# Kernel tuning notes

Hardware: AMD Instinct MI355X
Metric: run time of the kernel (lower is better)

Reference implementation:

```python
import jax, jax.numpy as jnp
import numpy as np

H = 768
L = 9
M = 5            # max_span_length
CTX_RATIO = 0.5
NEG_INF = -1e30


def setup_inputs() -> dict:
    key = jax.random.key(0)
    ks = jax.random.split(key, 12)
    B, S = 4, 2048
    sc = 1.0 / np.sqrt(H)
    return {
        "sequence_output": jax.random.normal(ks[0], (B, S, H), dtype=jnp.float32),
        "Wc": jax.random.normal(ks[1], (H, L), dtype=jnp.float32) * sc,
        "bc": jnp.zeros((L,), dtype=jnp.float32),
        "wa": jax.random.normal(ks[2], (H,), dtype=jnp.float32) * sc,
        "ba": jnp.zeros((), dtype=jnp.float32),
        "W1": jax.random.normal(ks[3], (2 * H, H), dtype=jnp.float32) * (1.0 / np.sqrt(2 * H)),
        "b1": jnp.zeros((H,), dtype=jnp.float32),
        "gamma": jnp.ones((H,), dtype=jnp.float32),
        "beta": jnp.zeros((H,), dtype=jnp.float32),
        "W2": jax.random.normal(ks[4], (H, L), dtype=jnp.float32) * sc,
        "b2": jnp.zeros((L,), dtype=jnp.float32),
    }


def reference(sequence_output, Wc, bc, wa, ba, W1, b1, gamma, beta, W2, b2):
    x = sequence_output                        # [B,S,H]
    B, S, _ = x.shape
    base_logits = jnp.einsum('bsh,hl->bsl', x, Wc) + bc   # [B,S,L]

    # sliding-window indices: window [i-M, i+M] clipped to [0, S)
    offsets = jnp.arange(-M, M + 1)            # [W]
    idx = jnp.arange(S)[:, None] + offsets     # [S,W]
    valid = (idx >= 0) & (idx < S)             # [S,W]
    idx_c = jnp.clip(idx, 0, S - 1)            # [S,W]

    # attention scores over window (span_attention linear -> scalar per token)
    scores = jnp.einsum('bsh,h->bs', x, wa) + ba           # [B,S]
    win_scores = scores[:, idx_c]                          # [B,S,W]
    win_scores = jnp.where(valid[None], win_scores, NEG_INF)
    attn = jax.nn.softmax(win_scores, axis=-1)             # [B,S,W]

    win_tokens = x[:, idx_c]                               # [B,S,W,H] gather
    weighted_ctx = jnp.einsum('bsw,bswh->bsh', attn, win_tokens)

    token_with_ctx = jnp.concatenate([x, weighted_ctx], axis=-1)  # [B,S,2H]
    h = jnp.einsum('bsd,dh->bsh', token_with_ctx, W1) + b1
    # LayerNorm (eps = 1e-5, torch default)
    mu = jnp.mean(h, axis=-1, keepdims=True)
    var = jnp.mean((h - mu) ** 2, axis=-1, keepdims=True)
    h = (h - mu) * jax.lax.rsqrt(var + 1e-5) * gamma + beta
    h = jax.nn.gelu(h, approximate=False)                  # torch nn.GELU default (erf)
    ctx_logits = jnp.einsum('bsh,hl->bsl', h, W2) + b2

    return (1.0 - CTX_RATIO) * base_logits + CTX_RATIO * ctx_logits
```

## Files before the change

### kernel.cpp

```cpp
#include <hip/hip_runtime.h>
#include <hip/hip_bf16.h>
#include <math.h>

#define S_LEN 2048
#define BATCH 4
#define HDIM 768
#define LOUT 9
#define NROWS (BATCH*S_LEN)
#define K2H 1536
#define WIN 11
#define NEG_INF_F (-1e30f)

typedef __attribute__((ext_vector_type(4))) float f32x4;
typedef __attribute__((ext_vector_type(8))) short bf16x8;

static __device__ __forceinline__ void async_ld16(const void* g, void* l) {
  __builtin_amdgcn_global_load_lds((const __attribute__((address_space(1))) void*)g,
                                   (__attribute__((address_space(3))) void*)l, 16, 0, 0);
}

static __device__ __forceinline__ unsigned short f2bf(float f) {
  union { float f; unsigned int u; } v; v.f = f;
  unsigned int u = v.u;
  unsigned int r = (u + 0x7fffu + ((u >> 16) & 1u)) >> 16;
  return (unsigned short)r;
}

__global__ __launch_bounds__(192) void k_prep(const float* __restrict__ x,
                                              const float* __restrict__ wa,
                                              const float* __restrict__ ba,
                                              unsigned short* __restrict__ xc,
                                              float* __restrict__ scores) {
  __shared__ float red[3];
  int row = blockIdx.x;
  int t = threadIdx.x;
  int lane = t & 63, wave = t >> 6;
  const float4 v = *(const float4*)(x + row * HDIM + t * 4);
  const float4 w = *(const float4*)(wa + t * 4);
  ushort4 o;
  o.x = f2bf(v.x); o.y = f2bf(v.y); o.z = f2bf(v.z); o.w = f2bf(v.w);
  *(ushort4*)(xc + row * K2H + t * 4) = o;
  float p = v.x * w.x + v.y * w.y + v.z * w.z + v.w * w.w;
  #pragma unroll
  for (int m = 1; m < 64; m <<= 1) p += __shfl_xor(p, m);
  if (lane == 0) red[wave] = p;
  __syncthreads();
  if (t == 0) scores[row] = red[0] + red[1] + red[2] + ba[0];
}

__global__ __launch_bounds__(256) void k_prep_w1t(const float* __restrict__ W1,
                                                  unsigned short* __restrict__ W1t) {
  __shared__ float tile[32][33];
  int bk = blockIdx.x % 48;
  int bn = blockIdx.x / 48;
  int tc = threadIdx.x % 32;
  int tr = threadIdx.x / 32;
  #pragma unroll
  for (int i = 0; i < 32; i += 8) {
    tile[tr + i][tc] = W1[(bk*32 + tr + i) * HDIM + bn*32 + tc];
  }
  __syncthreads();
  #pragma unroll
  for (int i = 0; i < 32; i += 8) {
    W1t[(bn*32 + tr + i) * K2H + bk*32 + tc] = f2bf(tile[tc][tr + i]);
  }
}

__global__ __launch_bounds__(256) void k_ctx(const float* __restrict__ x,
                                             const float* __restrict__ scores,
                                             const float* __restrict__ Wc,
                                             const float* __restrict__ bc,
                                             unsigned short* __restrict__ xc,
                                             float* __restrict__ base) {
  __shared__ float scl[WIN];
  __shared__ float es[WIN];
  __shared__ int rowidx[WIN];
  __shared__ float red[4][LOUT];
  int row = blockIdx.x;
  int b = row >> 11, s = row & 2047;
  int t = threadIdx.x;
  if (t < WIN) {
    int j = s - 5 + t;
    bool valid = (j >= 0) && (j < S_LEN);
    int jc = valid ? j : (j < 0 ? 0 : S_LEN - 1);
    rowidx[t] = b * S_LEN + jc;
    scl[t] = valid ? scores[b * S_LEN + jc] : NEG_INF_F;
  }
  __syncthreads();
  float mx = scl[0];
  #pragma unroll
  for (int w = 1; w < WIN; ++w) mx = fmaxf(mx, scl[w]);
  if (t < WIN) {
    float sv = scl[t];
    es[t] = (sv > -1e29f) ? __expf(sv - mx) : 0.f;
  }
  __syncthreads();
  float ssum = 0.f;
  #pragma unroll
  for (int w = 0; w < WIN; ++w) ssum += es[w];
  float inv = 1.f / ssum;
  float acc0 = 0.f, acc1 = 0.f, acc2 = 0.f;
  #pragma unroll
  for (int w = 0; w < WIN; ++w) {
    float aw = es[w] * inv;
    const float* xr = x + rowidx[w] * HDIM;
    acc0 += aw * xr[t];
    acc1 += aw * xr[t + 256];
    acc2 += aw * xr[t + 512];
  }
  unsigned short* dst = xc + row * K2H + HDIM;
  dst[t]       = f2bf(acc0);
  dst[t + 256] = f2bf(acc1);
  dst[t + 512] = f2bf(acc2);
  const float* xr = x + row * HDIM;
  float p[LOUT] = {};
  #pragma unroll
  for (int i = 0; i < 3; ++i) {
    int e = t + i * 256;
    float xv = xr[e];
    const float* wrow = Wc + e * LOUT;
    #pragma unroll
    for (int l = 0; l < LOUT; ++l) p[l] += xv * wrow[l];
  }
  #pragma unroll
  for (int l = 0; l < LOUT; ++l) {
    #pragma unroll
    for (int m = 1; m < 64; m <<= 1) p[l] += __shfl_xor(p[l], m);
  }
  int lane = t & 63, wave = t >> 6;
  if (lane == 0) {
    #pragma unroll
    for (int l = 0; l < LOUT; ++l) red[wave][l] = p[l];
  }
  __syncthreads();
  if (t < LOUT) {
    base[row * LOUT + t] = red[0][t] + red[1][t] + red[2][t] + red[3][t] + bc[t];
  }
}

__global__ __launch_bounds__(256) void k_gemm(const unsigned short* __restrict__ A,
                                              const unsigned short* __restrict__ Bt,
                                              const float* __restrict__ b1,
                                              float* __restrict__ Hout) {
  __shared__ unsigned short As[2][128 * 64];
  __shared__ unsigned short Bs[2][64 * 64];
  int bid = blockIdx.x;
  int obid = (bid & 7) * 96 + (bid >> 3);
  int bm = obid / 12, bn = obid % 12;
  int t = threadIdx.x;
  int lane = t & 63, wave = t >> 6;
  int rsub = lane >> 3;
  int kslot = lane & 7;

  int aRow0 = bm * 128 + (wave * 4 + 0) * 8 + rsub;
  int bRow0 = bn * 64  + (wave * 2 + 0) * 8 + rsub;
  const unsigned short* gA = A  + aRow0 * K2H + kslot * 8;
  const unsigned short* gB = Bt + bRow0 * K2H + kslot * 8;

  f32x4 acc[2][4] = {};
  int laneRow = lane & 15;
  int laneK = (lane >> 4) * 8;
  const unsigned short* aBase0 = &As[0][(wave * 32 + laneRow) * 64 + laneK];
  const unsigned short* bBase0 = &Bs[0][laneRow * 64 + laneK];

#define STAGE(buf, kt) do {                                                   \
    _Pragma("unroll")                                                         \
    for (int j = 0; j < 4; ++j)                                               \
      async_ld16(gA + j * 8 * K2H + (kt), &As[buf][(wave * 4 + j) * 512]);    \
    _Pragma("unroll")                                                         \
    for (int j = 0; j < 2; ++j)                                               \
      async_ld16(gB + j * 8 * K2H + (kt), &Bs[buf][(wave * 2 + j) * 512]);    \
  } while (0)

#define COMPUTE(buf) do {                                                     \
    const unsigned short* aB = aBase0 + (buf) * 128 * 64;                     \
    const unsigned short* bB = bBase0 + (buf) * 64 * 64;                      \
    _Pragma("unroll")                                                         \
    for (int kk = 0; kk < 2; ++kk) {                                          \
      bf16x8 af[2], bf[4];                                                    \
      _Pragma("unroll")                                                       \
      for (int m = 0; m < 2; ++m) af[m] = *(const bf16x8*)(aB + m*16*64 + kk*32); \
      _Pragma("unroll")                                                       \
      for (int n = 0; n < 4; ++n) bf[n] = *(const bf16x8*)(bB + n*16*64 + kk*32); \
      _Pragma("unroll")                                                       \
      for (int m = 0; m < 2; ++m)                                             \
        _Pragma("unroll")                                                     \
        for (int n = 0; n < 4; ++n)                                           \
          acc[m][n] = __builtin_amdgcn_mfma_f32_16x16x32_bf16(af[m], bf[n], acc[m][n], 0, 0, 0); \
    }                                                                         \
  } while (0)

  STAGE(0, 0);
  __syncthreads();
  int cur = 0;
  for (int kt = 64; kt < K2H; kt += 64) {
    STAGE(cur ^ 1, kt);
    COMPUTE(cur);
    __syncthreads();
    cur ^= 1;
  }
  COMPUTE(cur);

  int orow = bm * 128 + wave * 32 + (lane >> 4) * 4;
  int ocol = bn * 64 + (lane & 15);
  #pragma unroll
  for (int m = 0; m < 2; ++m)
    #pragma unroll
    for (int n = 0; n < 4; ++n) {
      int col = ocol + n * 16;
      float bv = b1[col];
      #pragma unroll
      for (int r = 0; r < 4; ++r) {
        Hout[(orow + m * 16 + r) * HDIM + col] = acc[m][n][r] + bv;
      }
    }
#undef STAGE
#undef COMPUTE
}

__global__ __launch_bounds__(256) void k_ln(const float* __restrict__ Hin,
                                            const float* __restrict__ gamma,
                                            const float* __restrict__ beta,
                                            const float* __restrict__ W2,
                                            const float* __restrict__ b2,
                                            const float* __restrict__ base,
                                            float* __restrict__ out) {
  __shared__ float redS[4], redQ[4], redp[4][LOUT];
  int row = blockIdx.x;
  int t = threadIdx.x;
  int lane = t & 63, wave = t >> 6;
  const float* hr = Hin + row * HDIM;
  float v0 = hr[t], v1 = hr[t + 256], v2 = hr[t + 512];
  float s1 = v0 + v1 + v2;
  float s2 = v0 * v0 + v1 * v1 + v2 * v2;
  #pragma unroll
  for (int m = 1; m < 64; m <<= 1) { s1 += __shfl_xor(s1, m); s2 += __shfl_xor(s2, m); }
  if (lane == 0) { redS[wave] = s1; redQ[wave] = s2; }
  __syncthreads();
  s1 = redS[0] + redS[1] + redS[2] + redS[3];
  s2 = redQ[0] + redQ[1] + redQ[2] + redQ[3];
  float mu = s1 * (1.f / HDIM);
  float var = s2 * (1.f / HDIM) - mu * mu;
  float rstd = rsqrtf(var + 1e-5f);
  float p[LOUT] = {};
  float vv[3] = { v0, v1, v2 };
  #pragma unroll
  for (int i = 0; i < 3; ++i) {
    int e = t + i * 256;
    float g = (vv[i] - mu) * rstd * gamma[e] + beta[e];
    float gg = 0.5f * g * (1.f + erff(g * 0.70710678118654752f));
    const float* wrow = W2 + e * LOUT;
    #pragma unroll
    for (int l = 0; l < LOUT; ++l) p[l] += gg * wrow[l];
  }
  #pragma unroll
  for (int l = 0; l < LOUT; ++l) {
    #pragma unroll
    for (int m = 1; m < 64; m <<= 1) p[l] += __shfl_xor(p[l], m);
  }
  if (lane == 0) {
    #pragma unroll
    for (int l = 0; l < LOUT; ++l) redp[wave][l] = p[l];
  }
  __syncthreads();
  if (t < LOUT) {
    float cl = redp[0][t] + redp[1][t] + redp[2][t] + redp[3][t] + b2[t];
    out[row * LOUT + t] = 0.5f * base[row * LOUT + t] + 0.5f * cl;
  }
}

extern "C" void kernel_launch(void* const* d_in, const int* in_sizes, int n_in,
                              void* d_out, int out_size, void* d_ws, size_t ws_size,
                              hipStream_t stream) {
  const float* x     = (const float*)d_in[0];
  const float* Wc    = (const float*)d_in[1];
  const float* bc    = (const float*)d_in[2];
  const float* wa    = (const float*)d_in[3];
  const float* ba    = (const float*)d_in[4];
  const float* W1    = (const float*)d_in[5];
  const float* b1    = (const float*)d_in[6];
  const float* gamma = (const float*)d_in[7];
  const float* beta  = (const float*)d_in[8];
  const float* W2    = (const float*)d_in[9];
  const float* b2    = (const float*)d_in[10];
  float* out = (float*)d_out;

  char* ws = (char*)d_ws;
  unsigned short* xc  = (unsigned short*)(ws);
  unsigned short* w1t = (unsigned short*)(ws + 25165824);
  float* scores       = (float*)(ws + 27525120);
  float* base         = (float*)(ws + 27557888);
  float* hbuf         = (float*)(ws + 27852800);

  k_prep    <<<dim3(8192), dim3(192), 0, stream>>>(x, wa, ba, xc, scores);
  k_prep_w1t<<<dim3(1152), dim3(256), 0, stream>>>(W1, w1t);
  k_ctx     <<<dim3(8192), dim3(256), 0, stream>>>(x, scores, Wc, bc, xc, base);
  k_gemm    <<<dim3(768),  dim3(256), 0, stream>>>(xc, w1t, b1, hbuf);
  k_ln      <<<dim3(8192), dim3(256), 0, stream>>>(hbuf, gamma, beta, W2, b2, base, out);
}
```

Measured before the change: 194.5 us.

## Fuse score computation into context kernel and retile GEMM with swizzled K=32 stages

Removes the separate prep kernel by having each context block recompute the window attention scores from its 11 loaded rows and also write the bf16 copy of x. This drops a launch and the scores round trip, at the cost of redundant dot products (11x per row) and cross-wave reductions. The GEMM now stages K in 32-wide chunks with an XOR-swizzled LDS layout to avoid bank conflicts. Halving the LDS footprint with launch bounds of 4 blocks per CU aims for higher occupancy, but the K loop now runs twice as many iterations with a barrier each.

```diff
diff --git a/kernel.cpp b/kernel.cpp
--- a/kernel.cpp
+++ b/kernel.cpp
@@ -26,28 +26,6 @@
   return (unsigned short)r;
 }
 
-__global__ __launch_bounds__(192) void k_prep(const float* __restrict__ x,
-                                              const float* __restrict__ wa,
-                                              const float* __restrict__ ba,
-                                              unsigned short* __restrict__ xc,
-                                              float* __restrict__ scores) {
-  __shared__ float red[3];
-  int row = blockIdx.x;
-  int t = threadIdx.x;
-  int lane = t & 63, wave = t >> 6;
-  const float4 v = *(const float4*)(x + row * HDIM + t * 4);
-  const float4 w = *(const float4*)(wa + t * 4);
-  ushort4 o;
-  o.x = f2bf(v.x); o.y = f2bf(v.y); o.z = f2bf(v.z); o.w = f2bf(v.w);
-  *(ushort4*)(xc + row * K2H + t * 4) = o;
-  float p = v.x * w.x + v.y * w.y + v.z * w.z + v.w * w.w;
-  #pragma unroll
-  for (int m = 1; m < 64; m <<= 1) p += __shfl_xor(p, m);
-  if (lane == 0) red[wave] = p;
-  __syncthreads();
-  if (t == 0) scores[row] = red[0] + red[1] + red[2] + ba[0];
-}
-
 __global__ __launch_bounds__(256) void k_prep_w1t(const float* __restrict__ W1,
                                                   unsigned short* __restrict__ W1t) {
   __shared__ float tile[32][33];
@@ -67,133 +45,155 @@
 }
 
 __global__ __launch_bounds__(256) void k_ctx(const float* __restrict__ x,
-                                             const float* __restrict__ scores,
+                                             const float* __restrict__ wa,
+                                             const float* __restrict__ ba,
                                              const float* __restrict__ Wc,
                                              const float* __restrict__ bc,
                                              unsigned short* __restrict__ xc,
                                              float* __restrict__ base) {
-  __shared__ float scl[WIN];
-  __shared__ float es[WIN];
-  __shared__ int rowidx[WIN];
-  __shared__ float red[4][LOUT];
+  __shared__ float sred[4][WIN];
+  __shared__ float redp[4][LOUT];
   int row = blockIdx.x;
   int b = row >> 11, s = row & 2047;
   int t = threadIdx.x;
-  if (t < WIN) {
-    int j = s - 5 + t;
+  int lane = t & 63, wave = t >> 6;
+
+  float xv[WIN][3];
+  bool vld[WIN];
+  #pragma unroll
+  for (int w = 0; w < WIN; ++w) {
+    int j = s - 5 + w;
     bool valid = (j >= 0) && (j < S_LEN);
+    vld[w] = valid;
     int jc = valid ? j : (j < 0 ? 0 : S_LEN - 1);
-    rowidx[t] = b * S_LEN + jc;
-    scl[t] = valid ? scores[b * S_LEN + jc] : NEG_INF_F;
-  }
-  __syncthreads();
-  float mx = scl[0];
-  #pragma unroll
-  for (int w = 1; w < WIN; ++w) mx = fmaxf(mx, scl[w]);
-  if (t < WIN) {
-    float sv = scl[t];
-    es[t] = (sv > -1e29f) ? __expf(sv - mx) : 0.f;
-  }
-  __syncthreads();
-  float ssum = 0.f;
-  #pragma unroll
-  for (int w = 0; w < WIN; ++w) ssum += es[w];
+    const float* xr = x + (b * S_LEN + jc) * HDIM;
+    xv[w][0] = xr[t];
+    xv[w][1] = xr[t + 256];
+    xv[w][2] = xr[t + 512];
+  }
+  float wa0 = wa[t], wa1 = wa[t + 256], wa2 = wa[t + 512];
+
+  float sp[WIN];
+  #pragma unroll
+  for (int w = 0; w < WIN; ++w)
+    sp[w] = xv[w][0] * wa0 + xv[w][1] * wa1 + xv[w][2] * wa2;
+  #pragma unroll
+  for (int w = 0; w < WIN; ++w)
+    #pragma unroll
+    for (int m = 1; m < 64; m <<= 1) sp[w] += __shfl_xor(sp[w], m);
+  if (lane == 0) {
+    #pragma unroll
+    for (int w = 0; w < WIN; ++w) sred[wave][w] = sp[w];
+  }
+  __syncthreads();
+  float bav = ba[0];
+  float sc[WIN];
+  #pragma unroll
+  for (int w = 0; w < WIN; ++w) {
+    float v = sred[0][w] + sred[1][w] + sred[2][w] + sred[3][w] + bav;
+    sc[w] = vld[w] ? v : NEG_INF_F;
+  }
+  float mx = sc[0];
+  #pragma unroll
+  for (int w = 1; w < WIN; ++w) mx = fmaxf(mx, sc[w]);
+  float es[WIN], ssum = 0.f;
+  #pragma unroll
+  for (int w = 0; w < WIN; ++w) {
+    es[w] = vld[w] ? __expf(sc[w] - mx) : 0.f;
+    ssum += es[w];
+  }
   float inv = 1.f / ssum;
-  float acc0 = 0.f, acc1 = 0.f, acc2 = 0.f;
+
+  float c0 = 0.f, c1 = 0.f, c2 = 0.f;
   #pragma unroll
   for (int w = 0; w < WIN; ++w) {
     float aw = es[w] * inv;
-    const float* xr = x + rowidx[w] * HDIM;
-    acc0 += aw * xr[t];
-    acc1 += aw * xr[t + 256];
-    acc2 += aw * xr[t + 512];
-  }
-  unsigned short* dst = xc + row * K2H + HDIM;
-  dst[t]       = f2bf(acc0);
-  dst[t + 256] = f2bf(acc1);
-  dst[t + 512] = f2bf(acc2);
-  const float* xr = x + row * HDIM;
+    c0 += aw * xv[w][0];
+    c1 += aw * xv[w][1];
+    c2 += aw * xv[w][2];
+  }
+  unsigned short* dstc = xc + row * K2H;
+  dstc[t]       = f2bf(xv[5][0]);
+  dstc[t + 256] = f2bf(xv[5][1]);
+  dstc[t + 512] = f2bf(xv[5][2]);
+  dstc[HDIM + t]       = f2bf(c0);
+  dstc[HDIM + t + 256] = f2bf(c1);
+  dstc[HDIM + t + 512] = f2bf(c2);
+
   float p[LOUT] = {};
   #pragma unroll
   for (int i = 0; i < 3; ++i) {
     int e = t + i * 256;
-    float xv = xr[e];
+    float xvv = xv[5][i];
     const float* wrow = Wc + e * LOUT;
     #pragma unroll
-    for (int l = 0; l < LOUT; ++l) p[l] += xv * wrow[l];
-  }
-  #pragma unroll
-  for (int l = 0; l < LOUT; ++l) {
+    for (int l = 0; l < LOUT; ++l) p[l] += xvv * wrow[l];
+  }
+  #pragma unroll
+  for (int l = 0; l < LOUT; ++l)
     #pragma unroll
     for (int m = 1; m < 64; m <<= 1) p[l] += __shfl_xor(p[l], m);
-  }
-  int lane = t & 63, wave = t >> 6;
   if (lane == 0) {
     #pragma unroll
-    for (int l = 0; l < LOUT; ++l) red[wave][l] = p[l];
+    for (int l = 0; l < LOUT; ++l) redp[wave][l] = p[l];
   }
   __syncthreads();
   if (t < LOUT) {
-    base[row * LOUT + t] = red[0][t] + red[1][t] + red[2][t] + red[3][t] + bc[t];
-  }
-}
-
-__global__ __launch_bounds__(256) void k_gemm(const unsigned short* __restrict__ A,
-                                              const unsigned short* __restrict__ Bt,
-                                              const float* __restrict__ b1,
-                                              float* __restrict__ Hout) {
-  __shared__ unsigned short As[2][128 * 64];
-  __shared__ unsigned short Bs[2][64 * 64];
+    base[row * LOUT + t] = redp[0][t] + redp[1][t] + redp[2][t] + redp[3][t] + bc[t];
+  }
+}
+
+__global__ __launch_bounds__(256, 4) void k_gemm(const unsigned short* __restrict__ A,
+                                                 const unsigned short* __restrict__ Bt,
+                                                 const float* __restrict__ b1,
+                                                 float* __restrict__ Hout) {
+  __shared__ unsigned short As[2][128 * 32];
+  __shared__ unsigned short Bs[2][64 * 32];
   int bid = blockIdx.x;
   int obid = (bid & 7) * 96 + (bid >> 3);
   int bm = obid / 12, bn = obid % 12;
   int t = threadIdx.x;
   int lane = t & 63, wave = t >> 6;
-  int rsub = lane >> 3;
-  int kslot = lane & 7;
-
-  int aRow0 = bm * 128 + (wave * 4 + 0) * 8 + rsub;
-  int bRow0 = bn * 64  + (wave * 2 + 0) * 8 + rsub;
-  const unsigned short* gA = A  + aRow0 * K2H + kslot * 8;
-  const unsigned short* gB = Bt + bRow0 * K2H + kslot * 8;
+
+  int fl = ((lane >> 2) ^ (lane >> 4)) & 3;
+  int sSrc = ((lane & 3) ^ fl);
+  int rIn = lane >> 2;
+
+  const unsigned short* gA = A  + (bm * 128 + wave * 32 + rIn) * K2H + sSrc * 8;
+  const unsigned short* gB = Bt + (bn * 64  + wave * 16 + rIn) * K2H + sSrc * 8;
 
   f32x4 acc[2][4] = {};
+
   int laneRow = lane & 15;
-  int laneK = (lane >> 4) * 8;
-  const unsigned short* aBase0 = &As[0][(wave * 32 + laneRow) * 64 + laneK];
-  const unsigned short* bBase0 = &Bs[0][laneRow * 64 + laneK];
-
-#define STAGE(buf, kt) do {                                                   \
-    _Pragma("unroll")                                                         \
-    for (int j = 0; j < 4; ++j)                                               \
-      async_ld16(gA + j * 8 * K2H + (kt), &As[buf][(wave * 4 + j) * 512]);    \
-    _Pragma("unroll")                                                         \
-    for (int j = 0; j < 2; ++j)                                               \
-      async_ld16(gB + j * 8 * K2H + (kt), &Bs[buf][(wave * 2 + j) * 512]);    \
+  int slot = lane >> 4;
+  int fr = ((lane & 3) ^ ((lane >> 2) & 3));
+  int rdOff = ((slot ^ fr) & 3) * 8;
+
+#define STAGE(buf, kt) do {                                                    \
+    async_ld16(gA + (kt),             &As[buf][(wave * 32) * 32]);             \
+    async_ld16(gA + 16 * K2H + (kt),  &As[buf][(wave * 32 + 16) * 32]);        \
+    async_ld16(gB + (kt),             &Bs[buf][(wave * 16) * 32]);             \
   } while (0)
 
-#define COMPUTE(buf) do {                                                     \
-    const unsigned short* aB = aBase0 + (buf) * 128 * 64;                     \
-    const unsigned short* bB = bBase0 + (buf) * 64 * 64;                      \
-    _Pragma("unroll")                                                         \
-    for (int kk = 0; kk < 2; ++kk) {                                          \
-      bf16x8 af[2], bf[4];                                                    \
-      _Pragma("unroll")                                                       \
-      for (int m = 0; m < 2; ++m) af[m] = *(const bf16x8*)(aB + m*16*64 + kk*32); \
-      _Pragma("unroll")                                                       \
-      for (int n = 0; n < 4; ++n) bf[n] = *(const bf16x8*)(bB + n*16*64 + kk*32); \
-      _Pragma("unroll")                                                       \
-      for (int m = 0; m < 2; ++m)                                             \
-        _Pragma("unroll")                                                     \
-        for (int n = 0; n < 4; ++n)                                           \
-          acc[m][n] = __builtin_amdgcn_mfma_f32_16x16x32_bf16(af[m], bf[n], acc[m][n], 0, 0, 0); \
-    }                                                                         \
+#define COMPUTE(buf) do {                                                      \
+    bf16x8 af[2], bfv[4];                                                      \
+    _Pragma("unroll")                                                          \
+    for (int m = 0; m < 2; ++m)                                                \
+      af[m] = *(const bf16x8*)(&As[buf][(wave * 32 + m * 16 + laneRow) * 32 + rdOff]); \
+    _Pragma("unroll")                                                          \
+    for (int n = 0; n < 4; ++n)                                                \
+      bfv[n] = *(const bf16x8*)(&Bs[buf][(n * 16 + laneRow) * 32 + rdOff]);    \
+    _Pragma("unroll")                                                          \
+    for (int m = 0; m < 2; ++m)                                                \
+      _Pragma("unroll")                                                        \
+      for (int n = 0; n < 4; ++n)                                              \
+        acc[m][n] = __builtin_amdgcn_mfma_f32_16x16x32_bf16(af[m], bfv[n], acc[m][n], 0, 0, 0); \
   } while (0)
 
   STAGE(0, 0);
   __syncthreads();
   int cur = 0;
-  for (int kt = 64; kt < K2H; kt += 64) {
+  for (int kt = 32; kt < K2H; kt += 32) {
     STAGE(cur ^ 1, kt);
     COMPUTE(cur);
     __syncthreads();
@@ -254,10 +254,9 @@
     for (int l = 0; l < LOUT; ++l) p[l] += gg * wrow[l];
   }
   #pragma unroll
-  for (int l = 0; l < LOUT; ++l) {
+  for (int l = 0; l < LOUT; ++l)
     #pragma unroll
     for (int m = 1; m < 64; m <<= 1) p[l] += __shfl_xor(p[l], m);
-  }
   if (lane == 0) {
     #pragma unroll
     for (int l = 0; l < LOUT; ++l) redp[wave][l] = p[l];
@@ -288,13 +287,11 @@
   char* ws = (char*)d_ws;
   unsigned short* xc  = (unsigned short*)(ws);
   unsigned short* w1t = (unsigned short*)(ws + 25165824);
-  float* scores       = (float*)(ws + 27525120);
-  float* base         = (float*)(ws + 27557888);
-  float* hbuf         = (float*)(ws + 27852800);
-
-  k_prep    <<<dim3(8192), dim3(192), 0, stream>>>(x, wa, ba, xc, scores);
+  float* base         = (float*)(ws + 27525120);
+  float* hbuf         = (float*)(ws + 27820032);
+
   k_prep_w1t<<<dim3(1152), dim3(256), 0, stream>>>(W1, w1t);
-  k_ctx     <<<dim3(8192), dim3(256), 0, stream>>>(x, scores, Wc, bc, xc, base);
+  k_ctx     <<<dim3(8192), dim3(256), 0, stream>>>(x, wa, ba, Wc, bc, xc, base);
   k_gemm    <<<dim3(768),  dim3(256), 0, stream>>>(xc, w1t, b1, hbuf);
   k_ln      <<<dim3(8192), dim3(256), 0, stream>>>(hbuf, gamma, beta, W2, b2, base, out);
 }
```

After: 205.3 us. 5.6% more time.
